# Performance work log

Hardware: AMD Instinct MI355X
Metric: run time of the kernel (lower is better)

Reference implementation:

```python
import jax, jax.numpy as jnp
import numpy as np

N_NODES = 50000
N_EDGES = 640000
IN_CH = 128
OUT_CH = 128
HID = 2 * OUT_CH  # 256


def _glorot(key, shape):
    fan_in, fan_out = shape
    lim = np.sqrt(6.0 / (fan_in + fan_out)).astype(np.float32)
    return jax.random.uniform(key, shape, jnp.float32, -lim, lim)


def setup_inputs() -> dict:
    key = jax.random.key(0)
    ks = jax.random.split(key, 8)
    x = jax.random.normal(ks[0], (N_NODES, IN_CH), jnp.float32)
    edge_index = jax.random.randint(ks[1], (2, N_EDGES), 0, N_NODES, jnp.int64)
    # SAGEConv layer 1: lin_l (neighbor branch, with bias), lin_r (root branch, no bias)
    w1_l = _glorot(ks[2], (IN_CH, HID))
    b1_l = jnp.zeros((HID,), jnp.float32)
    w1_r = _glorot(ks[3], (IN_CH, HID))
    # SAGEConv layer 2
    w2_l = _glorot(ks[4], (HID, OUT_CH))
    b2_l = jnp.zeros((OUT_CH,), jnp.float32)
    w2_r = _glorot(ks[5], (HID, OUT_CH))
    return {"x": x, "edge_index": edge_index,
            "w1_l": w1_l, "b1_l": b1_l, "w1_r": w1_r,
            "w2_l": w2_l, "b2_l": b2_l, "w2_r": w2_r}


def _sage_conv(x, src, dst, w_l, b_l, w_r):
    # mean aggregation of source-node features onto destination nodes
    msgs = x[src]                                       # [E, C] gather
    agg = jax.ops.segment_sum(msgs, dst, num_segments=N_NODES)  # [N, C]
    cnt = jax.ops.segment_sum(jnp.ones((src.shape[0],), x.dtype), dst,
                              num_segments=N_NODES)     # [N]
    mean = agg / jnp.maximum(cnt, 1.0)[:, None]
    # out = lin_l(mean_neighbors) + lin_r(x_root)
    return mean @ w_l + b_l + x @ w_r


def reference(x, edge_index, w1_l, b1_l, w1_r, w2_l, b2_l, w2_r):
    src, dst = edge_index[0], edge_index[1]
    h = _sage_conv(x, src, dst, w1_l, b1_l, w1_r)
    h = jax.nn.relu(h)
    return _sage_conv(h, src, dst, w2_l, b2_l, w2_r)
```

## Files before the change

### kernel.cpp

```cpp
#include <hip/hip_runtime.h>

#define N_NODES 50000
#define N_EDGES 640000
#define IN_CH 128
#define OUT_CH 128
#define HID 256
#define M_PAD 50048
#define CAP 48

typedef unsigned int uint;
typedef unsigned short ushort;

__device__ __forceinline__ ushort f2b(float f) {
    uint u = __float_as_uint(f);
    u += 0x7FFFu + ((u >> 16) & 1u);
    return (ushort)(u >> 16);
}
__device__ __forceinline__ float b2f_lo(uint u) { return __uint_as_float(u << 16); }
__device__ __forceinline__ float b2f_hi(uint u) { return __uint_as_float(u & 0xFFFF0000u); }
__device__ __forceinline__ uint packb(float lo, float hi) {
    return (uint)f2b(lo) | ((uint)f2b(hi) << 16);
}

__device__ __forceinline__ void gload_lds16(const ushort* g, ushort* l) {
    __builtin_amdgcn_global_load_lds(
        (const __attribute__((address_space(1))) void*)g,
        (__attribute__((address_space(3))) void*)l, 16, 0, 0);
}

__global__ __launch_bounds__(256) void prep_edges(
    const int* __restrict__ src, const int* __restrict__ dst,
    int* __restrict__ cnt, ushort* __restrict__ col) {
    int base = (blockIdx.x * 256 + threadIdx.x) * 4;
    int4 d4 = *(const int4*)(dst + base);
    int4 s4 = *(const int4*)(src + base);
    int p0 = atomicAdd(&cnt[d4.x], 1);
    int p1 = atomicAdd(&cnt[d4.y], 1);
    int p2 = atomicAdd(&cnt[d4.z], 1);
    int p3 = atomicAdd(&cnt[d4.w], 1);
    if (p0 < CAP) col[d4.x * CAP + p0] = (ushort)s4.x;
    if (p1 < CAP) col[d4.y * CAP + p1] = (ushort)s4.y;
    if (p2 < CAP) col[d4.z * CAP + p2] = (ushort)s4.z;
    if (p3 < CAP) col[d4.w * CAP + p3] = (ushort)s4.w;
}

__global__ __launch_bounds__(256) void prep_cast(
    const float* __restrict__ x, const float* __restrict__ w1l,
    const float* __restrict__ w1r, const float* __restrict__ w2l,
    const float* __restrict__ w2r, ushort* __restrict__ xcat,
    ushort* __restrict__ w1f, ushort* __restrict__ w2f) {
    int id = blockIdx.x * 256 + threadIdx.x;
    if (id < 800000) {
        long long base = (long long)id * 8;
        float4 a = *(const float4*)(x + base);
        float4 c = *(const float4*)(x + base + 4);
        uint4 o;
        o.x = packb(a.x, a.y);
        o.y = packb(a.z, a.w);
        o.z = packb(c.x, c.y);
        o.w = packb(c.z, c.w);
        int row = id >> 4;
        int cc = id & 15;
        ((uint4*)xcat)[(size_t)row * 32 + 16 + cc] = o;
    } else if (id < 865536) {
        int i = id - 800000;
        int n0 = i >> 12, kk = (i >> 9) & 7, lane = (i >> 3) & 63, j = i & 7;
        int n = n0 * 16 + (lane & 15);
        int k = kk * 32 + (lane >> 4) * 8 + j;
        float v = (k < 128) ? w1l[k * 256 + n] : w1r[(k - 128) * 256 + n];
        w1f[i] = f2b(v);
    } else {
        int i = id - 865536;
        int n0 = i >> 12, kk = (i >> 9) & 7, lane = (i >> 3) & 63, j = i & 7;
        int n = n0 * 16 + (lane & 15);
        int k = kk * 32 + (lane >> 4) * 8 + j;
        float v = (n < 128) ? w2l[k * 128 + n] : w2r[k * 128 + (n - 128)];
        w2f[i] = f2b(v);
    }
}

__global__ __launch_bounds__(256) void aggregate_mean1(
    const int* __restrict__ cnt, const ushort* __restrict__ col,
    ushort* __restrict__ xcat) {
    int t = blockIdx.x * 256 + threadIdx.x;
    int node = t >> 4;
    int q = t & 15;
    if (node >= N_NODES) return;
    int degf = cnt[node];
    int deg = min(degf, CAP);
    const ushort* cb = col + node * CAP;
    float acc[8] = {0.f, 0.f, 0.f, 0.f, 0.f, 0.f, 0.f, 0.f};
    const uint4* f4 = (const uint4*)xcat;
    int j = 0;
    for (; j + 8 <= deg; j += 8) {
        uint4 c4 = *(const uint4*)(cb + j);
        int s0 = c4.x & 0xFFFF, s1 = c4.x >> 16;
        int s2 = c4.y & 0xFFFF, s3 = c4.y >> 16;
        int s4 = c4.z & 0xFFFF, s5 = c4.z >> 16;
        int s6 = c4.w & 0xFFFF, s7 = c4.w >> 16;
        uint4 v0 = f4[(size_t)s0 * 32 + 16 + q];
        uint4 v1 = f4[(size_t)s1 * 32 + 16 + q];
        uint4 v2 = f4[(size_t)s2 * 32 + 16 + q];
        uint4 v3 = f4[(size_t)s3 * 32 + 16 + q];
        uint4 v4 = f4[(size_t)s4 * 32 + 16 + q];
        uint4 v5 = f4[(size_t)s5 * 32 + 16 + q];
        uint4 v6 = f4[(size_t)s6 * 32 + 16 + q];
        uint4 v7 = f4[(size_t)s7 * 32 + 16 + q];
        acc[0] += b2f_lo(v0.x) + b2f_lo(v1.x) + b2f_lo(v2.x) + b2f_lo(v3.x)
                + b2f_lo(v4.x) + b2f_lo(v5.x) + b2f_lo(v6.x) + b2f_lo(v7.x);
        acc[1] += b2f_hi(v0.x) + b2f_hi(v1.x) + b2f_hi(v2.x) + b2f_hi(v3.x)
                + b2f_hi(v4.x) + b2f_hi(v5.x) + b2f_hi(v6.x) + b2f_hi(v7.x);
        acc[2] += b2f_lo(v0.y) + b2f_lo(v1.y) + b2f_lo(v2.y) + b2f_lo(v3.y)
                + b2f_lo(v4.y) + b2f_lo(v5.y) + b2f_lo(v6.y) + b2f_lo(v7.y);
        acc[3] += b2f_hi(v0.y) + b2f_hi(v1.y) + b2f_hi(v2.y) + b2f_hi(v3.y)
                + b2f_hi(v4.y) + b2f_hi(v5.y) + b2f_hi(v6.y) + b2f_hi(v7.y);
        acc[4] += b2f_lo(v0.z) + b2f_lo(v1.z) + b2f_lo(v2.z) + b2f_lo(v3.z)
                + b2f_lo(v4.z) + b2f_lo(v5.z) + b2f_lo(v6.z) + b2f_lo(v7.z);
        acc[5] += b2f_hi(v0.z) + b2f_hi(v1.z) + b2f_hi(v2.z) + b2f_hi(v3.z)
                + b2f_hi(v4.z) + b2f_hi(v5.z) + b2f_hi(v6.z) + b2f_hi(v7.z);
        acc[6] += b2f_lo(v0.w) + b2f_lo(v1.w) + b2f_lo(v2.w) + b2f_lo(v3.w)
                + b2f_lo(v4.w) + b2f_lo(v5.w) + b2f_lo(v6.w) + b2f_lo(v7.w);
        acc[7] += b2f_hi(v0.w) + b2f_hi(v1.w) + b2f_hi(v2.w) + b2f_hi(v3.w)
                + b2f_hi(v4.w) + b2f_hi(v5.w) + b2f_hi(v6.w) + b2f_hi(v7.w);
    }
    for (; j < deg; ++j) {
        uint4 v = f4[(size_t)cb[j] * 32 + 16 + q];
        acc[0] += b2f_lo(v.x); acc[1] += b2f_hi(v.x);
        acc[2] += b2f_lo(v.y); acc[3] += b2f_hi(v.y);
        acc[4] += b2f_lo(v.z); acc[5] += b2f_hi(v.z);
        acc[6] += b2f_lo(v.w); acc[7] += b2f_hi(v.w);
    }
    float inv = 1.0f / fmaxf((float)degf, 1.0f);
    uint4 o;
    o.x = packb(acc[0] * inv, acc[1] * inv);
    o.y = packb(acc[2] * inv, acc[3] * inv);
    o.z = packb(acc[4] * inv, acc[5] * inv);
    o.w = packb(acc[6] * inv, acc[7] * inv);
    ((uint4*)xcat)[(size_t)node * 32 + q] = o;
}

__global__ __launch_bounds__(256) void combine2(
    const ushort* __restrict__ hw, const int* __restrict__ cnt,
    const ushort* __restrict__ col, const float* __restrict__ bias,
    float* __restrict__ out) {
    int t = blockIdx.x * 256 + threadIdx.x;
    int node = t >> 4;
    int q = t & 15;
    if (node >= N_NODES) return;
    int degf = cnt[node];
    int deg = min(degf, CAP);
    const ushort* cb = col + node * CAP;
    float acc[8] = {0.f, 0.f, 0.f, 0.f, 0.f, 0.f, 0.f, 0.f};
    const uint4* f4 = (const uint4*)hw;
    int j = 0;
    for (; j + 8 <= deg; j += 8) {
        uint4 c4 = *(const uint4*)(cb + j);
        int s0 = c4.x & 0xFFFF, s1 = c4.x >> 16;
        int s2 = c4.y & 0xFFFF, s3 = c4.y >> 16;
        int s4 = c4.z & 0xFFFF, s5 = c4.z >> 16;
        int s6 = c4.w & 0xFFFF, s7 = c4.w >> 16;
        uint4 v0 = f4[(size_t)s0 * 32 + q];
        uint4 v1 = f4[(size_t)s1 * 32 + q];
        uint4 v2 = f4[(size_t)s2 * 32 + q];
        uint4 v3 = f4[(size_t)s3 * 32 + q];
        uint4 v4 = f4[(size_t)s4 * 32 + q];
        uint4 v5 = f4[(size_t)s5 * 32 + q];
        uint4 v6 = f4[(size_t)s6 * 32 + q];
        uint4 v7 = f4[(size_t)s7 * 32 + q];
        acc[0] += b2f_lo(v0.x) + b2f_lo(v1.x) + b2f_lo(v2.x) + b2f_lo(v3.x)
                + b2f_lo(v4.x) + b2f_lo(v5.x) + b2f_lo(v6.x) + b2f_lo(v7.x);
        acc[1] += b2f_hi(v0.x) + b2f_hi(v1.x) + b2f_hi(v2.x) + b2f_hi(v3.x)
                + b2f_hi(v4.x) + b2f_hi(v5.x) + b2f_hi(v6.x) + b2f_hi(v7.x);
        acc[2] += b2f_lo(v0.y) + b2f_lo(v1.y) + b2f_lo(v2.y) + b2f_lo(v3.y)
                + b2f_lo(v4.y) + b2f_lo(v5.y) + b2f_lo(v6.y) + b2f_lo(v7.y);
        acc[3] += b2f_hi(v0.y) + b2f_hi(v1.y) + b2f_hi(v2.y) + b2f_hi(v3.y)
                + b2f_hi(v4.y) + b2f_hi(v5.y) + b2f_hi(v6.y) + b2f_hi(v7.y);
        acc[4] += b2f_lo(v0.z) + b2f_lo(v1.z) + b2f_lo(v2.z) + b2f_lo(v3.z)
                + b2f_lo(v4.z) + b2f_lo(v5.z) + b2f_lo(v6.z) + b2f_lo(v7.z);
        acc[5] += b2f_hi(v0.z) + b2f_hi(v1.z) + b2f_hi(v2.z) + b2f_hi(v3.z)
                + b2f_hi(v4.z) + b2f_hi(v5.z) + b2f_hi(v6.z) + b2f_hi(v7.z);
        acc[6] += b2f_lo(v0.w) + b2f_lo(v1.w) + b2f_lo(v2.w) + b2f_lo(v3.w)
                + b2f_lo(v4.w) + b2f_lo(v5.w) + b2f_lo(v6.w) + b2f_lo(v7.w);
        acc[7] += b2f_hi(v0.w) + b2f_hi(v1.w) + b2f_hi(v2.w) + b2f_hi(v3.w)
                + b2f_hi(v4.w) + b2f_hi(v5.w) + b2f_hi(v6.w) + b2f_hi(v7.w);
    }
    for (; j < deg; ++j) {
        uint4 v = f4[(size_t)cb[j] * 32 + q];
        acc[0] += b2f_lo(v.x); acc[1] += b2f_hi(v.x);
        acc[2] += b2f_lo(v.y); acc[3] += b2f_hi(v.y);
        acc[4] += b2f_lo(v.z); acc[5] += b2f_hi(v.z);
        acc[6] += b2f_lo(v.w); acc[7] += b2f_hi(v.w);
    }
    float inv = 1.0f / fmaxf((float)degf, 1.0f);
    uint4 r = f4[(size_t)node * 32 + 16 + q];
    float4 b0 = *(const float4*)(bias + q * 8);
    float4 b1 = *(const float4*)(bias + q * 8 + 4);
    float4 o0, o1;
    o0.x = acc[0] * inv + b2f_lo(r.x) + b0.x;
    o0.y = acc[1] * inv + b2f_hi(r.x) + b0.y;
    o0.z = acc[2] * inv + b2f_lo(r.y) + b0.z;
    o0.w = acc[3] * inv + b2f_hi(r.y) + b0.w;
    o1.x = acc[4] * inv + b2f_lo(r.z) + b1.x;
    o1.y = acc[5] * inv + b2f_hi(r.z) + b1.y;
    o1.z = acc[6] * inv + b2f_lo(r.w) + b1.z;
    o1.w = acc[7] * inv + b2f_hi(r.w) + b1.w;
    *(float4*)(out + (size_t)node * 128 + q * 8) = o0;
    *(float4*)(out + (size_t)node * 128 + q * 8 + 4) = o1;
}

using bf16x8 = __attribute__((ext_vector_type(8))) short;
using f32x4  = __attribute__((ext_vector_type(4))) float;

__global__ __launch_bounds__(256) void fused_gemm(
    const ushort* __restrict__ A, const ushort* __restrict__ w1f,
    const ushort* __restrict__ w2f, const float* __restrict__ b1,
    ushort* __restrict__ hw) {
    __shared__ alignas(16) ushort tile[64 * 256];

    const int tid = threadIdx.x;
    const int lane = tid & 63;
    const int wave = tid >> 6;
    const int quad = lane >> 4;
    const int l16 = lane & 15;
    const int bm = blockIdx.x * 64;

#pragma unroll
    for (int r = 0; r < 8; ++r) {
        int row = r * 8 + (tid >> 5);
        int c = tid & 31;
        int src = (c & 24) | ((c & 7) ^ (row & 7));
        gload_lds16(A + (size_t)(bm + row) * 256 + src * 8, &tile[row * 256 + c * 8]);
    }

    f32x4 acc[4][4];
#pragma unroll
    for (int rt = 0; rt < 4; ++rt)
#pragma unroll
        for (int ct = 0; ct < 4; ++ct) acc[rt][ct] = (f32x4){0.f, 0.f, 0.f, 0.f};

    const size_t bstep = 64 * 8;
    const ushort* w1b = w1f + (((size_t)(wave * 4) * 8) * 64 + lane) * 8;
    const ushort* w2b = w2f + (((size_t)(wave * 4) * 8) * 64 + lane) * 8;

    bf16x8 bp[2][4];
#pragma unroll
    for (int ct = 0; ct < 4; ++ct) {
        bp[0][ct] = *(const bf16x8*)(w1b + ((size_t)ct * 8 + 0) * bstep);
        bp[1][ct] = *(const bf16x8*)(w1b + ((size_t)ct * 8 + 1) * bstep);
    }

    __syncthreads();

#pragma unroll
    for (int kk = 0; kk < 8; ++kk) {
        bf16x8 bn[4];
        if (kk < 6) {
#pragma unroll
            for (int ct = 0; ct < 4; ++ct)
                bn[ct] = *(const bf16x8*)(w1b + ((size_t)ct * 8 + kk + 2) * bstep);
        }
        bf16x8 af[4];
#pragma unroll
        for (int rt = 0; rt < 4; ++rt) {
            int row = rt * 16 + l16;
            int c = kk * 4 + quad;
            int slot = (c & 24) | ((c & 7) ^ (row & 7));
            af[rt] = *(const bf16x8*)&tile[row * 256 + slot * 8];
        }
#pragma unroll
        for (int ct = 0; ct < 4; ++ct) {
#pragma unroll
            for (int rt = 0; rt < 4; ++rt)
                acc[rt][ct] = __builtin_amdgcn_mfma_f32_16x16x32_bf16(
                    af[rt], bp[kk & 1][ct], acc[rt][ct], 0, 0, 0);
        }
        if (kk < 6) {
#pragma unroll
            for (int ct = 0; ct < 4; ++ct) bp[kk & 1][ct] = bn[ct];
        }
    }
    __syncthreads();

#pragma unroll
    for (int ct = 0; ct < 4; ++ct) {
        bp[0][ct] = *(const bf16x8*)(w2b + ((size_t)ct * 8 + 0) * bstep);
        bp[1][ct] = *(const bf16x8*)(w2b + ((size_t)ct * 8 + 1) * bstep);
    }

#pragma unroll
    for (int ct = 0; ct < 4; ++ct) {
        int colg = wave * 64 + ct * 16 + l16;
        float bv = b1[colg];
        int cc = colg >> 3;
        int off = colg & 7;
#pragma unroll
        for (int rt = 0; rt < 4; ++rt) {
#pragma unroll
            for (int reg = 0; reg < 4; ++reg) {
                int row = rt * 16 + quad * 4 + reg;
                int slot = (cc & 24) | ((cc & 7) ^ (row & 7));
                tile[row * 256 + slot * 8 + off] = f2b(fmaxf(acc[rt][ct][reg] + bv, 0.0f));
            }
        }
    }

#pragma unroll
    for (int rt = 0; rt < 4; ++rt)
#pragma unroll
        for (int ct = 0; ct < 4; ++ct) acc[rt][ct] = (f32x4){0.f, 0.f, 0.f, 0.f};

    __syncthreads();

#pragma unroll
    for (int kk = 0; kk < 8; ++kk) {
        bf16x8 bn[4];
        if (kk < 6) {
#pragma unroll
            for (int ct = 0; ct < 4; ++ct)
                bn[ct] = *(const bf16x8*)(w2b + ((size_t)ct * 8 + kk + 2) * bstep);
        }
        bf16x8 af[4];
#pragma unroll
        for (int rt = 0; rt < 4; ++rt) {
            int row = rt * 16 + l16;
            int c = kk * 4 + quad;
            int slot = (c & 24) | ((c & 7) ^ (row & 7));
            af[rt] = *(const bf16x8*)&tile[row * 256 + slot * 8];
        }
#pragma unroll
        for (int ct = 0; ct < 4; ++ct) {
#pragma unroll
            for (int rt = 0; rt < 4; ++rt)
                acc[rt][ct] = __builtin_amdgcn_mfma_f32_16x16x32_bf16(
                    af[rt], bp[kk & 1][ct], acc[rt][ct], 0, 0, 0);
        }
        if (kk < 6) {
#pragma unroll
            for (int ct = 0; ct < 4; ++ct) bp[kk & 1][ct] = bn[ct];
        }
    }
    __syncthreads();

#pragma unroll
    for (int ct = 0; ct < 4; ++ct) {
        int colg = wave * 64 + ct * 16 + l16;
        int cc = colg >> 3;
        int off = colg & 7;
#pragma unroll
        for (int rt = 0; rt < 4; ++rt) {
#pragma unroll
            for (int reg = 0; reg < 4; ++reg) {
                int row = rt * 16 + quad * 4 + reg;
                int slot = (cc & 24) | ((cc & 7) ^ (row & 7));
                tile[row * 256 + slot * 8 + off] = f2b(acc[rt][ct][reg]);
            }
        }
    }
    __syncthreads();
#pragma unroll
    for (int r = 0; r < 8; ++r) {
        int row = r * 8 + (tid >> 5);
        int c = tid & 31;
        int slot = (c & 24) | ((c & 7) ^ (row & 7));
        uint4 v = *(const uint4*)&tile[row * 256 + slot * 8];
        *(uint4*)(hw + (size_t)(bm + row) * 256 + c * 8) = v;
    }
}

extern "C" void kernel_launch(void* const* d_in, const int* in_sizes, int n_in,
                              void* d_out, int out_size, void* d_ws, size_t ws_size,
                              hipStream_t stream) {
    const float* x    = (const float*)d_in[0];
    const int*   ei   = (const int*)d_in[1];
    const float* w1_l = (const float*)d_in[2];
    const float* b1_l = (const float*)d_in[3];
    const float* w1_r = (const float*)d_in[4];
    const float* w2_l = (const float*)d_in[5];
    const float* b2_l = (const float*)d_in[6];
    const float* w2_r = (const float*)d_in[7];
    float* out = (float*)d_out;

    const int* src = ei;
    const int* dst = ei + N_EDGES;

    int* cnt = (int*)d_ws;
    ushort* col = (ushort*)(cnt + N_NODES);
    size_t ib = (size_t)N_NODES * 4 + (size_t)N_NODES * CAP * 2;
    size_t ofs = (ib + 15) & ~(size_t)15;
    ushort* xcat = (ushort*)((char*)d_ws + ofs);
    ushort* hw   = xcat + (size_t)M_PAD * HID;
    ushort* w1f  = hw + (size_t)M_PAD * HID;
    ushort* w2f  = w1f + HID * HID;

    hipMemsetAsync(cnt, 0, (size_t)N_NODES * sizeof(int), stream);

    prep_edges<<<625, 256, 0, stream>>>(src, dst, cnt, col);
    prep_cast<<<3637, 256, 0, stream>>>(x, w1_l, w1_r, w2_l, w2_r, xcat, w1f, w2f);

    aggregate_mean1<<<N_NODES * 16 / 256, 256, 0, stream>>>(cnt, col, xcat);
    fused_gemm<<<M_PAD / 64, 256, 0, stream>>>(xcat, w1f, w2f, b1_l, hw);
    combine2<<<N_NODES * 16 / 256, 256, 0, stream>>>(hw, cnt, col, b2_l, out);
}
```

Measured before the change: 236.1 us.

## Make fused GEMM persistent with double-buffered async A-tile prefetch

The fused GEMM now launches a fixed grid of 512 blocks, each handling up to two 64-row chunks. The next chunk's A tile is loaded into a second LDS buffer while the current chunk computes. The goal is to hide global-load latency and cut the tail from 782 short-lived blocks. The cost is double the LDS (64KB), which may lower occupancy, and uneven work, since only some blocks get a second chunk.

Result: slower. 251.2 us (+6.4%).

```diff
diff --git a/kernel.cpp b/kernel.cpp
--- a/kernel.cpp
+++ b/kernel.cpp
@@ -6,6 +6,8 @@
 #define OUT_CH 128
 #define HID 256
 #define M_PAD 50048
+#define NCHUNK 782
+#define GEMM_GRID 512
 #define CAP 48
 
 typedef unsigned int uint;
@@ -215,155 +217,180 @@
     const ushort* __restrict__ A, const ushort* __restrict__ w1f,
     const ushort* __restrict__ w2f, const float* __restrict__ b1,
     ushort* __restrict__ hw) {
-    __shared__ alignas(16) ushort tile[64 * 256];
+    __shared__ alignas(16) ushort Abuf[2][64 * 256];
 
     const int tid = threadIdx.x;
     const int lane = tid & 63;
     const int wave = tid >> 6;
     const int quad = lane >> 4;
     const int l16 = lane & 15;
-    const int bm = blockIdx.x * 64;
-
-#pragma unroll
-    for (int r = 0; r < 8; ++r) {
-        int row = r * 8 + (tid >> 5);
-        int c = tid & 31;
-        int src = (c & 24) | ((c & 7) ^ (row & 7));
-        gload_lds16(A + (size_t)(bm + row) * 256 + src * 8, &tile[row * 256 + c * 8]);
-    }
-
-    f32x4 acc[4][4];
-#pragma unroll
-    for (int rt = 0; rt < 4; ++rt)
-#pragma unroll
-        for (int ct = 0; ct < 4; ++ct) acc[rt][ct] = (f32x4){0.f, 0.f, 0.f, 0.f};
+
+    const int srow = tid >> 5;
+    const int sc = tid & 31;
+    const int ssrc = (sc & 24) | ((sc & 7) ^ (srow & 7));
 
     const size_t bstep = 64 * 8;
     const ushort* w1b = w1f + (((size_t)(wave * 4) * 8) * 64 + lane) * 8;
     const ushort* w2b = w2f + (((size_t)(wave * 4) * 8) * 64 + lane) * 8;
 
-    bf16x8 bp[2][4];
-#pragma unroll
-    for (int ct = 0; ct < 4; ++ct) {
-        bp[0][ct] = *(const bf16x8*)(w1b + ((size_t)ct * 8 + 0) * bstep);
-        bp[1][ct] = *(const bf16x8*)(w1b + ((size_t)ct * 8 + 1) * bstep);
-    }
-
-    __syncthreads();
-
-#pragma unroll
-    for (int kk = 0; kk < 8; ++kk) {
-        bf16x8 bn[4];
-        if (kk < 6) {
-#pragma unroll
-            for (int ct = 0; ct < 4; ++ct)
-                bn[ct] = *(const bf16x8*)(w1b + ((size_t)ct * 8 + kk + 2) * bstep);
-        }
-        bf16x8 af[4];
-#pragma unroll
-        for (int rt = 0; rt < 4; ++rt) {
-            int row = rt * 16 + l16;
-            int c = kk * 4 + quad;
-            int slot = (c & 24) | ((c & 7) ^ (row & 7));
-            af[rt] = *(const bf16x8*)&tile[row * 256 + slot * 8];
-        }
+    {
+        const ushort* gb = A + (size_t)(blockIdx.x * 64) * 256;
+#pragma unroll
+        for (int r = 0; r < 8; ++r) {
+            int row = r * 8 + srow;
+            gload_lds16(gb + (size_t)row * 256 + ssrc * 8,
+                        &Abuf[0][row * 256 + sc * 8]);
+        }
+    }
+
+    for (int ci = 0; ci < 2; ++ci) {
+        int chunk = blockIdx.x + ci * GEMM_GRID;
+        if (chunk >= NCHUNK) break;
+        ushort* tile = Abuf[ci & 1];
+        const int bm = chunk * 64;
+
+        __syncthreads();
+
+        int nchunk = blockIdx.x + (ci + 1) * GEMM_GRID;
+        if (nchunk < NCHUNK) {
+            ushort* ntile = Abuf[(ci & 1) ^ 1];
+            const ushort* gb = A + (size_t)nchunk * 64 * 256;
+#pragma unroll
+            for (int r = 0; r < 8; ++r) {
+                int row = r * 8 + srow;
+                gload_lds16(gb + (size_t)row * 256 + ssrc * 8,
+                            &ntile[row * 256 + sc * 8]);
+            }
+        }
+
+        f32x4 acc[4][4];
+#pragma unroll
+        for (int rt = 0; rt < 4; ++rt)
+#pragma unroll
+            for (int ct = 0; ct < 4; ++ct) acc[rt][ct] = (f32x4){0.f, 0.f, 0.f, 0.f};
+
+        bf16x8 bp[2][4];
 #pragma unroll
         for (int ct = 0; ct < 4; ++ct) {
-#pragma unroll
-            for (int rt = 0; rt < 4; ++rt)
-                acc[rt][ct] = __builtin_amdgcn_mfma_f32_16x16x32_bf16(
-                    af[rt], bp[kk & 1][ct], acc[rt][ct], 0, 0, 0);
-        }
-        if (kk < 6) {
-#pragma unroll
-            for (int ct = 0; ct < 4; ++ct) bp[kk & 1][ct] = bn[ct];
-        }
-    }
-    __syncthreads();
-
-#pragma unroll
-    for (int ct = 0; ct < 4; ++ct) {
-        bp[0][ct] = *(const bf16x8*)(w2b + ((size_t)ct * 8 + 0) * bstep);
-        bp[1][ct] = *(const bf16x8*)(w2b + ((size_t)ct * 8 + 1) * bstep);
-    }
-
-#pragma unroll
-    for (int ct = 0; ct < 4; ++ct) {
-        int colg = wave * 64 + ct * 16 + l16;
-        float bv = b1[colg];
-        int cc = colg >> 3;
-        int off = colg & 7;
-#pragma unroll
-        for (int rt = 0; rt < 4; ++rt) {
-#pragma unroll
-            for (int reg = 0; reg < 4; ++reg) {
-                int row = rt * 16 + quad * 4 + reg;
-                int slot = (cc & 24) | ((cc & 7) ^ (row & 7));
-                tile[row * 256 + slot * 8 + off] = f2b(fmaxf(acc[rt][ct][reg] + bv, 0.0f));
-            }
-        }
-    }
-
-#pragma unroll
-    for (int rt = 0; rt < 4; ++rt)
-#pragma unroll
-        for (int ct = 0; ct < 4; ++ct) acc[rt][ct] = (f32x4){0.f, 0.f, 0.f, 0.f};
-
-    __syncthreads();
-
-#pragma unroll
-    for (int kk = 0; kk < 8; ++kk) {
-        bf16x8 bn[4];
-        if (kk < 6) {
-#pragma unroll
-            for (int ct = 0; ct < 4; ++ct)
-                bn[ct] = *(const bf16x8*)(w2b + ((size_t)ct * 8 + kk + 2) * bstep);
-        }
-        bf16x8 af[4];
-#pragma unroll
-        for (int rt = 0; rt < 4; ++rt) {
-            int row = rt * 16 + l16;
-            int c = kk * 4 + quad;
-            int slot = (c & 24) | ((c & 7) ^ (row & 7));
-            af[rt] = *(const bf16x8*)&tile[row * 256 + slot * 8];
-        }
+            bp[0][ct] = *(const bf16x8*)(w1b + ((size_t)ct * 8 + 0) * bstep);
+            bp[1][ct] = *(const bf16x8*)(w1b + ((size_t)ct * 8 + 1) * bstep);
+        }
+
+#pragma unroll
+        for (int kk = 0; kk < 8; ++kk) {
+            bf16x8 bn[4];
+            if (kk < 6) {
+#pragma unroll
+                for (int ct = 0; ct < 4; ++ct)
+                    bn[ct] = *(const bf16x8*)(w1b + ((size_t)ct * 8 + kk + 2) * bstep);
+            }
+            bf16x8 af[4];
+#pragma unroll
+            for (int rt = 0; rt < 4; ++rt) {
+                int row = rt * 16 + l16;
+                int c = kk * 4 + quad;
+                int slot = (c & 24) | ((c & 7) ^ (row & 7));
+                af[rt] = *(const bf16x8*)&tile[row * 256 + slot * 8];
+            }
+#pragma unroll
+            for (int ct = 0; ct < 4; ++ct) {
+#pragma unroll
+                for (int rt = 0; rt < 4; ++rt)
+                    acc[rt][ct] = __builtin_amdgcn_mfma_f32_16x16x32_bf16(
+                        af[rt], bp[kk & 1][ct], acc[rt][ct], 0, 0, 0);
+            }
+            if (kk < 6) {
+#pragma unroll
+                for (int ct = 0; ct < 4; ++ct) bp[kk & 1][ct] = bn[ct];
+            }
+        }
+
+        __syncthreads();
+
 #pragma unroll
         for (int ct = 0; ct < 4; ++ct) {
-#pragma unroll
-            for (int rt = 0; rt < 4; ++rt)
-                acc[rt][ct] = __builtin_amdgcn_mfma_f32_16x16x32_bf16(
-                    af[rt], bp[kk & 1][ct], acc[rt][ct], 0, 0, 0);
-        }
-        if (kk < 6) {
-#pragma unroll
-            for (int ct = 0; ct < 4; ++ct) bp[kk & 1][ct] = bn[ct];
-        }
-    }
-    __syncthreads();
-
-#pragma unroll
-    for (int ct = 0; ct < 4; ++ct) {
-        int colg = wave * 64 + ct * 16 + l16;
-        int cc = colg >> 3;
-        int off = colg & 7;
-#pragma unroll
-        for (int rt = 0; rt < 4; ++rt) {
-#pragma unroll
-            for (int reg = 0; reg < 4; ++reg) {
-                int row = rt * 16 + quad * 4 + reg;
-                int slot = (cc & 24) | ((cc & 7) ^ (row & 7));
-                tile[row * 256 + slot * 8 + off] = f2b(acc[rt][ct][reg]);
-            }
-        }
-    }
-    __syncthreads();
-#pragma unroll
-    for (int r = 0; r < 8; ++r) {
-        int row = r * 8 + (tid >> 5);
-        int c = tid & 31;
-        int slot = (c & 24) | ((c & 7) ^ (row & 7));
-        uint4 v = *(const uint4*)&tile[row * 256 + slot * 8];
-        *(uint4*)(hw + (size_t)(bm + row) * 256 + c * 8) = v;
+            int colg = wave * 64 + ct * 16 + l16;
+            float bv = b1[colg];
+            int cc = colg >> 3;
+            int off = colg & 7;
+#pragma unroll
+            for (int rt = 0; rt < 4; ++rt) {
+#pragma unroll
+                for (int reg = 0; reg < 4; ++reg) {
+                    int row = rt * 16 + quad * 4 + reg;
+                    int slot = (cc & 24) | ((cc & 7) ^ (row & 7));
+                    tile[row * 256 + slot * 8 + off] =
+                        f2b(fmaxf(acc[rt][ct][reg] + bv, 0.0f));
+                }
+            }
+        }
+
+#pragma unroll
+        for (int rt = 0; rt < 4; ++rt)
+#pragma unroll
+            for (int ct = 0; ct < 4; ++ct) acc[rt][ct] = (f32x4){0.f, 0.f, 0.f, 0.f};
+
+#pragma unroll
+        for (int ct = 0; ct < 4; ++ct) {
+            bp[0][ct] = *(const bf16x8*)(w2b + ((size_t)ct * 8 + 0) * bstep);
+            bp[1][ct] = *(const bf16x8*)(w2b + ((size_t)ct * 8 + 1) * bstep);
+        }
+
+        __syncthreads();
+
+#pragma unroll
+        for (int kk = 0; kk < 8; ++kk) {
+            bf16x8 bn[4];
+            if (kk < 6) {
+#pragma unroll
+                for (int ct = 0; ct < 4; ++ct)
+                    bn[ct] = *(const bf16x8*)(w2b + ((size_t)ct * 8 + kk + 2) * bstep);
+            }
+            bf16x8 af[4];
+#pragma unroll
+            for (int rt = 0; rt < 4; ++rt) {
+                int row = rt * 16 + l16;
+                int c = kk * 4 + quad;
+                int slot = (c & 24) | ((c & 7) ^ (row & 7));
+                af[rt] = *(const bf16x8*)&tile[row * 256 + slot * 8];
+            }
+#pragma unroll
+            for (int ct = 0; ct < 4; ++ct) {
+#pragma unroll
+                for (int rt = 0; rt < 4; ++rt)
+                    acc[rt][ct] = __builtin_amdgcn_mfma_f32_16x16x32_bf16(
+                        af[rt], bp[kk & 1][ct], acc[rt][ct], 0, 0, 0);
+            }
+            if (kk < 6) {
+#pragma unroll
+                for (int ct = 0; ct < 4; ++ct) bp[kk & 1][ct] = bn[ct];
+            }
+        }
+
+        __syncthreads();
+
+#pragma unroll
+        for (int ct = 0; ct < 4; ++ct) {
+            int colg = wave * 64 + ct * 16 + l16;
+            int cc = colg >> 3;
+            int off = colg & 7;
+#pragma unroll
+            for (int rt = 0; rt < 4; ++rt) {
+#pragma unroll
+                for (int reg = 0; reg < 4; ++reg) {
+                    int row = rt * 16 + quad * 4 + reg;
+                    int slot = (cc & 24) | ((cc & 7) ^ (row & 7));
+                    tile[row * 256 + slot * 8 + off] = f2b(acc[rt][ct][reg]);
+                }
+            }
+        }
+        __syncthreads();
+#pragma unroll
+        for (int r = 0; r < 8; ++r) {
+            int row = r * 8 + srow;
+            uint4 v = *(const uint4*)&tile[row * 256 + ssrc * 8];
+            *(uint4*)(hw + (size_t)(bm + row) * 256 + sc * 8) = v;
+        }
     }
 }
 
@@ -398,6 +425,6 @@
     prep_cast<<<3637, 256, 0, stream>>>(x, w1_l, w1_r, w2_l, w2_r, xcat, w1f, w2f);
 
     aggregate_mean1<<<N_NODES * 16 / 256, 256, 0, stream>>>(cnt, col, xcat);
-    fused_gemm<<<M_PAD / 64, 256, 0, stream>>>(xcat, w1f, w2f, b1_l, hw);
+    fused_gemm<<<GEMM_GRID, 256, 0, stream>>>(xcat, w1f, w2f, b1_l, hw);
     combine2<<<N_NODES * 16 / 256, 256, 0, stream>>>(hw, cnt, col, b2_l, out);
 }
```
